# Kernel tuning notes

Measured on AMD Instinct MI355X. Metric: run time of the kernel, lower is better.

Reference implementation:

```python
import jax, jax.numpy as jnp
import numpy as np

N_NODES = 100000
N_EDGES = 3200000
D_IN = 128
D_H0 = 64
D_H1 = 32
N_GRAPHS = 1024
N_CLASSES = 16


def setup_inputs() -> dict:
    key = jax.random.key(0)
    ks = jax.random.split(key, 9)
    x = jax.random.normal(ks[0], (N_NODES, D_IN), dtype=jnp.float32)
    edge_index = jax.random.randint(ks[1], (2, N_EDGES), 0, N_NODES, dtype=jnp.int64)
    node_graph_index = jnp.sort(
        jax.random.randint(ks[2], (N_NODES,), 0, N_GRAPHS, dtype=jnp.int64))

    def glorot(k, shape):
        lim = np.sqrt(6.0 / (shape[0] + shape[1]))
        return jax.random.uniform(k, shape, jnp.float32, -lim, lim)

    W0 = glorot(ks[3], (D_IN, D_H0))
    b0 = jnp.zeros((D_H0,), jnp.float32)
    W1 = glorot(ks[4], (D_H0, D_H1))
    b1 = jnp.zeros((D_H1,), jnp.float32)
    Wd = glorot(ks[5], (D_H1, N_CLASSES))
    bd = jnp.zeros((N_CLASSES,), jnp.float32)
    return {"x": x, "edge_index": edge_index, "node_graph_index": node_graph_index,
            "W0": W0, "b0": b0, "W1": W1, "b1": b1, "Wd": Wd, "bd": bd}


def reference(x, edge_index, node_graph_index, W0, b0, W1, b1, Wd, bd):
    N = x.shape[0]
    # GCN renormalization: add self-loops, symmetric D^-1/2 (A+I) D^-1/2
    loops = jnp.arange(N, dtype=edge_index.dtype)
    row = jnp.concatenate([edge_index[0], loops])  # target nodes
    col = jnp.concatenate([edge_index[1], loops])  # source nodes
    deg = jax.ops.segment_sum(jnp.ones_like(row, dtype=x.dtype), row, num_segments=N)
    inv_sqrt = jax.lax.rsqrt(deg)  # deg >= 1 thanks to self-loops
    norm = inv_sqrt[row] * inv_sqrt[col]  # [E+N]

    def gcn(h, W, b):
        hW = h @ W                                   # [N, d_out]
        msg = hW[col] * norm[:, None]                # [E+N, d_out]
        agg = jax.ops.segment_sum(msg, row, num_segments=N)
        return jax.nn.relu(agg + b)

    h = gcn(x, W0, b0)          # [N, 64]  (dropout is identity at inference)
    h = gcn(h, W1, b1)          # [N, 32]

    # mean pool over graphs
    sums = jax.ops.segment_sum(h, node_graph_index, num_segments=N_GRAPHS)
    cnt = jax.ops.segment_sum(jnp.ones((N,), x.dtype), node_graph_index,
                              num_segments=N_GRAPHS)
    pooled = sums / jnp.maximum(cnt, 1.0)[:, None]   # [G, 32]
    return pooled @ Wd + bd                          # [G, n_classes]
```

## Files before the change

kernel.cpp:

```cpp
#include <hip/hip_runtime.h>

#define GSHIFT 8
#define GSIZE 256
#define MAXG 512
#define GCAP 8960
#define CHUNKA 8192

typedef unsigned short bfraw;

__device__ __forceinline__ bfraw f2bf(float f) {
    unsigned u = __float_as_uint(f);
    unsigned r = u + 0x7FFFu + ((u >> 16) & 1u);
    return (bfraw)(r >> 16);
}
__device__ __forceinline__ float bflo(unsigned u) { return __uint_as_float(u << 16); }
__device__ __forceinline__ float bfhi(unsigned u) { return __uint_as_float(u & 0xFFFF0000u); }


__global__ __launch_bounds__(512) void k_ginit(int* __restrict__ gcur, int ngroups) {
    int g = threadIdx.x;
    if (g < ngroups) gcur[g] = g * GCAP;
}

__global__ __launch_bounds__(512) void k_partA(const int* __restrict__ row,
                                               const int* __restrict__ col,
                                               int* __restrict__ gcur,
                                               int* __restrict__ gbuf,
                                               int E, int ngroups) {
    __shared__ int h[MAXG];
    __shared__ int lst[MAXG];
    __shared__ int base[MAXG];
    __shared__ int sorted[CHUNKA];
    __shared__ unsigned short gbin[CHUNKA];
    int tid = threadIdx.x;
    h[tid] = 0;
    int start = blockIdx.x * CHUNKA;
    int end = min(E, start + CHUNKA);
    int rr[16], cc[16];
#pragma unroll
    for (int q = 0; q < 4; ++q) {
        int i = start + tid * 4 + q * 2048;
        if (i + 3 < end) {
            int4 r4 = *(const int4*)(row + i);
            int4 c4 = *(const int4*)(col + i);
            rr[q * 4 + 0] = r4.x; rr[q * 4 + 1] = r4.y;
            rr[q * 4 + 2] = r4.z; rr[q * 4 + 3] = r4.w;
            cc[q * 4 + 0] = c4.x; cc[q * 4 + 1] = c4.y;
            cc[q * 4 + 2] = c4.z; cc[q * 4 + 3] = c4.w;
        } else {
#pragma unroll
            for (int j = 0; j < 4; ++j) {
                int idx = i + j;
                rr[q * 4 + j] = (idx < end) ? row[idx] : -1;
                cc[q * 4 + j] = (idx < end) ? col[idx] : 0;
            }
        }
    }
    __syncthreads();
#pragma unroll
    for (int j = 0; j < 16; ++j)
        if (rr[j] >= 0) atomicAdd(&h[rr[j] >> GSHIFT], 1);
    __syncthreads();
    int v = h[tid];
    lst[tid] = v;
    __syncthreads();
    for (int d = 1; d < MAXG; d <<= 1) {
        int a = (tid >= d) ? lst[tid - d] : 0;
        __syncthreads();
        lst[tid] += a;
        __syncthreads();
    }
    int excl = lst[tid] - v;
    base[tid] = (v > 0 && tid < ngroups) ? atomicAdd(&gcur[tid], v) : 0;
    lst[tid] = excl;
    h[tid] = excl;
    __syncthreads();
#pragma unroll
    for (int j = 0; j < 16; ++j) {
        int r = rr[j];
        if (r >= 0) {
            int g = r >> GSHIFT;
            int p = atomicAdd(&h[g], 1);
            sorted[p] = ((r & (GSIZE - 1)) << 17) | cc[j];
            gbin[p] = (unsigned short)g;
        }
    }
    __syncthreads();
    int cnt = end - start;
    for (int i = tid; i < cnt; i += 512) {
        int g = gbin[i];
        int dst = base[g] + (i - lst[g]);
        if (dst < (g + 1) * GCAP)
            gbuf[dst] = sorted[i];
    }
}

__global__ __launch_bounds__(512) void k_partB(const int* __restrict__ gbuf,
                                               const int* __restrict__ gcur,
                                               int* __restrict__ off,
                                               int* __restrict__ off2,
                                               int* __restrict__ scol,
                                               float* __restrict__ invs, int N) {
    __shared__ int hist[GSIZE];
    __shared__ int lex[GSIZE];
    __shared__ int sorted[GCAP];
    int g = blockIdx.x, tid = threadIdx.x;
    int s = g * GCAP;
    int cnt = min(gcur[g] - s, GCAP);
    if (tid < GSIZE) hist[tid] = 0;
    __syncthreads();
    for (int k = tid; k < cnt; k += 512)
        atomicAdd(&hist[gbuf[s + k] >> 17], 1);
    __syncthreads();
    int d0 = (tid < GSIZE) ? hist[tid] : 0;
    if (tid < GSIZE) lex[tid] = d0;
    __syncthreads();
    for (int d = 1; d < GSIZE; d <<= 1) {
        int a = 0;
        if (tid < GSIZE && tid >= d) a = lex[tid - d];
        __syncthreads();
        if (tid < GSIZE) lex[tid] += a;
        __syncthreads();
    }
    if (tid < GSIZE) {
        int excl = lex[tid] - d0;
        int node = (g << GSHIFT) + tid;
        if (node < N) {
            off[node] = s + excl;
            off2[node] = s + excl + d0;
            invs[node] = rsqrtf((float)(d0 + 1));
        }
        hist[tid] = excl;
    }
    __syncthreads();
    for (int k = tid; k < cnt; k += 512) {
        int p = gbuf[s + k];
        int pos = atomicAdd(&hist[p >> 17], 1);
        sorted[pos] = p & 0x1FFFF;
    }
    __syncthreads();
    for (int k = tid; k < cnt; k += 512) scol[s + k] = sorted[k];
}


__global__ __launch_bounds__(256) void k_gemm0(const float* __restrict__ x,
                                               const float* __restrict__ W,
                                               const float* __restrict__ invs,
                                               bfraw* __restrict__ out, int N) {
    __shared__ float sW[128 * 64];
    for (int i = threadIdx.x; i < 2048; i += 256)
        ((float4*)sW)[i] = ((const float4*)W)[i];
    __syncthreads();
    int t = threadIdx.x;
    int tc = t & 15, tr = t >> 4;
    int rbase = blockIdx.x * 64 + tr * 4;
    float acc[4][4] = {};
    int rr[4];
#pragma unroll
    for (int i = 0; i < 4; ++i) rr[i] = min(rbase + i, N - 1);
    for (int k = 0; k < 128; k += 4) {
        float4 wv0 = *(const float4*)&sW[(k + 0) * 64 + tc * 4];
        float4 wv1 = *(const float4*)&sW[(k + 1) * 64 + tc * 4];
        float4 wv2 = *(const float4*)&sW[(k + 2) * 64 + tc * 4];
        float4 wv3 = *(const float4*)&sW[(k + 3) * 64 + tc * 4];
#pragma unroll
        for (int i = 0; i < 4; ++i) {
            float4 xv = *(const float4*)(x + (size_t)rr[i] * 128 + k);
            acc[i][0] = fmaf(xv.x, wv0.x, acc[i][0]);
            acc[i][1] = fmaf(xv.x, wv0.y, acc[i][1]);
            acc[i][2] = fmaf(xv.x, wv0.z, acc[i][2]);
            acc[i][3] = fmaf(xv.x, wv0.w, acc[i][3]);
            acc[i][0] = fmaf(xv.y, wv1.x, acc[i][0]);
            acc[i][1] = fmaf(xv.y, wv1.y, acc[i][1]);
            acc[i][2] = fmaf(xv.y, wv1.z, acc[i][2]);
            acc[i][3] = fmaf(xv.y, wv1.w, acc[i][3]);
            acc[i][0] = fmaf(xv.z, wv2.x, acc[i][0]);
            acc[i][1] = fmaf(xv.z, wv2.y, acc[i][1]);
            acc[i][2] = fmaf(xv.z, wv2.z, acc[i][2]);
            acc[i][3] = fmaf(xv.z, wv2.w, acc[i][3]);
            acc[i][0] = fmaf(xv.w, wv3.x, acc[i][0]);
            acc[i][1] = fmaf(xv.w, wv3.y, acc[i][1]);
            acc[i][2] = fmaf(xv.w, wv3.z, acc[i][2]);
            acc[i][3] = fmaf(xv.w, wv3.w, acc[i][3]);
        }
    }
#pragma unroll
    for (int i = 0; i < 4; ++i) {
        int row = rbase + i;
        if (row < N) {
            float iv = invs[row];
            ushort4 o;
            o.x = f2bf(iv * acc[i][0]);
            o.y = f2bf(iv * acc[i][1]);
            o.z = f2bf(iv * acc[i][2]);
            o.w = f2bf(iv * acc[i][3]);
            *(ushort4*)(out + (size_t)row * 64 + tc * 4) = o;
        }
    }
}

__global__ __launch_bounds__(256) void k_gemm1(const float* __restrict__ h,
                                               const float* __restrict__ W,
                                               const float* __restrict__ invs,
                                               bfraw* __restrict__ out, int N) {
    __shared__ float sW[64 * 32];
    for (int i = threadIdx.x; i < 512; i += 256)
        ((float4*)sW)[i] = ((const float4*)W)[i];
    __syncthreads();
    int t = threadIdx.x;
    int tc = t & 7, tr = t >> 3;
    int rbase = blockIdx.x * 128 + tr * 4;
    float acc[4][4] = {};
    int rr[4];
#pragma unroll
    for (int i = 0; i < 4; ++i) rr[i] = min(rbase + i, N - 1);
    for (int k = 0; k < 64; k += 4) {
        float4 wv0 = *(const float4*)&sW[(k + 0) * 32 + tc * 4];
        float4 wv1 = *(const float4*)&sW[(k + 1) * 32 + tc * 4];
        float4 wv2 = *(const float4*)&sW[(k + 2) * 32 + tc * 4];
        float4 wv3 = *(const float4*)&sW[(k + 3) * 32 + tc * 4];
#pragma unroll
        for (int i = 0; i < 4; ++i) {
            float4 xv = *(const float4*)(h + (size_t)rr[i] * 64 + k);
            acc[i][0] = fmaf(xv.x, wv0.x, acc[i][0]);
            acc[i][1] = fmaf(xv.x, wv0.y, acc[i][1]);
            acc[i][2] = fmaf(xv.x, wv0.z, acc[i][2]);
            acc[i][3] = fmaf(xv.x, wv0.w, acc[i][3]);
            acc[i][0] = fmaf(xv.y, wv1.x, acc[i][0]);
            acc[i][1] = fmaf(xv.y, wv1.y, acc[i][1]);
            acc[i][2] = fmaf(xv.y, wv1.z, acc[i][2]);
            acc[i][3] = fmaf(xv.y, wv1.w, acc[i][3]);
            acc[i][0] = fmaf(xv.z, wv2.x, acc[i][0]);
            acc[i][1] = fmaf(xv.z, wv2.y, acc[i][1]);
            acc[i][2] = fmaf(xv.z, wv2.z, acc[i][2]);
            acc[i][3] = fmaf(xv.z, wv2.w, acc[i][3]);
            acc[i][0] = fmaf(xv.w, wv3.x, acc[i][0]);
            acc[i][1] = fmaf(xv.w, wv3.y, acc[i][1]);
            acc[i][2] = fmaf(xv.w, wv3.z, acc[i][2]);
            acc[i][3] = fmaf(xv.w, wv3.w, acc[i][3]);
        }
    }
#pragma unroll
    for (int i = 0; i < 4; ++i) {
        int row = rbase + i;
        if (row < N) {
            float iv = invs[row];
            ushort4 o;
            o.x = f2bf(iv * acc[i][0]);
            o.y = f2bf(iv * acc[i][1]);
            o.z = f2bf(iv * acc[i][2]);
            o.w = f2bf(iv * acc[i][3]);
            *(ushort4*)(out + (size_t)row * 32 + tc * 4) = o;
        }
    }
}


__global__ __launch_bounds__(256) void k_agg64_w(const int* __restrict__ scol,
                                                 const int* __restrict__ off,
                                                 const int* __restrict__ off2,
                                                 const float* __restrict__ invs,
                                                 const bfraw* __restrict__ hWb,
                                                 const float* __restrict__ bias,
                                                 float* __restrict__ h0, int N) {
    int node = blockIdx.x * 4 + (threadIdx.x >> 6);
    if (node >= N) return;
    int lane = threadIdx.x & 63;
    int fl = lane & 7, sg = lane >> 3;
    int s = off[node], e = off2[node];
    float a[8] = {}, c[8] = {};
    int k = s + sg;
    for (; k + 24 < e; k += 32) {
        int n0 = scol[k], n1 = scol[k + 8], n2 = scol[k + 16], n3 = scol[k + 24];
        uint4 u0 = *(const uint4*)(hWb + (size_t)n0 * 64 + fl * 8);
        uint4 u1 = *(const uint4*)(hWb + (size_t)n1 * 64 + fl * 8);
        uint4 u2 = *(const uint4*)(hWb + (size_t)n2 * 64 + fl * 8);
        uint4 u3 = *(const uint4*)(hWb + (size_t)n3 * 64 + fl * 8);
        a[0] += bflo(u0.x); a[1] += bfhi(u0.x); a[2] += bflo(u0.y); a[3] += bfhi(u0.y);
        a[4] += bflo(u0.z); a[5] += bfhi(u0.z); a[6] += bflo(u0.w); a[7] += bfhi(u0.w);
        c[0] += bflo(u1.x); c[1] += bfhi(u1.x); c[2] += bflo(u1.y); c[3] += bfhi(u1.y);
        c[4] += bflo(u1.z); c[5] += bfhi(u1.z); c[6] += bflo(u1.w); c[7] += bfhi(u1.w);
        a[0] += bflo(u2.x); a[1] += bfhi(u2.x); a[2] += bflo(u2.y); a[3] += bfhi(u2.y);
        a[4] += bflo(u2.z); a[5] += bfhi(u2.z); a[6] += bflo(u2.w); a[7] += bfhi(u2.w);
        c[0] += bflo(u3.x); c[1] += bfhi(u3.x); c[2] += bflo(u3.y); c[3] += bfhi(u3.y);
        c[4] += bflo(u3.z); c[5] += bfhi(u3.z); c[6] += bflo(u3.w); c[7] += bfhi(u3.w);
    }
    for (; k < e; k += 8) {
        uint4 u = *(const uint4*)(hWb + (size_t)scol[k] * 64 + fl * 8);
        a[0] += bflo(u.x); a[1] += bfhi(u.x); a[2] += bflo(u.y); a[3] += bfhi(u.y);
        a[4] += bflo(u.z); a[5] += bfhi(u.z); a[6] += bflo(u.w); a[7] += bfhi(u.w);
    }
#pragma unroll
    for (int j = 0; j < 8; ++j) a[j] += c[j];
#pragma unroll
    for (int m = 8; m < 64; m <<= 1) {
#pragma unroll
        for (int j = 0; j < 8; ++j) a[j] += __shfl_xor(a[j], m, 64);
    }
    if (sg == 0) {
        uint4 u = *(const uint4*)(hWb + (size_t)node * 64 + fl * 8);
        float iv = invs[node];
        int fb = fl * 8;
        float4 o1, o2;
        o1.x = fmaxf(iv * (a[0] + bflo(u.x)) + bias[fb + 0], 0.f);
        o1.y = fmaxf(iv * (a[1] + bfhi(u.x)) + bias[fb + 1], 0.f);
        o1.z = fmaxf(iv * (a[2] + bflo(u.y)) + bias[fb + 2], 0.f);
        o1.w = fmaxf(iv * (a[3] + bfhi(u.y)) + bias[fb + 3], 0.f);
        o2.x = fmaxf(iv * (a[4] + bflo(u.z)) + bias[fb + 4], 0.f);
        o2.y = fmaxf(iv * (a[5] + bfhi(u.z)) + bias[fb + 5], 0.f);
        o2.z = fmaxf(iv * (a[6] + bflo(u.w)) + bias[fb + 6], 0.f);
        o2.w = fmaxf(iv * (a[7] + bfhi(u.w)) + bias[fb + 7], 0.f);
        *(float4*)(h0 + (size_t)node * 64 + fb) = o1;
        *(float4*)(h0 + (size_t)node * 64 + fb + 4) = o2;
    }
}

__global__ __launch_bounds__(256) void k_agg32_w(const int* __restrict__ scol,
                                                 const int* __restrict__ off,
                                                 const int* __restrict__ off2,
                                                 const float* __restrict__ invs,
                                                 const bfraw* __restrict__ hWb,
                                                 const float* __restrict__ bias,
                                                 float* __restrict__ h1, int N) {
    int node = blockIdx.x * 4 + (threadIdx.x >> 6);
    if (node >= N) return;
    int lane = threadIdx.x & 63;
    int fl = lane & 3, sg = lane >> 2;
    int s = off[node], e = off2[node];
    float a[8] = {}, c[8] = {};
    int k = s + sg;
    for (; k + 16 < e; k += 32) {
        int n0 = scol[k], n1 = scol[k + 16];
        uint4 u0 = *(const uint4*)(hWb + (size_t)n0 * 32 + fl * 8);
        uint4 u1 = *(const uint4*)(hWb + (size_t)n1 * 32 + fl * 8);
        a[0] += bflo(u0.x); a[1] += bfhi(u0.x); a[2] += bflo(u0.y); a[3] += bfhi(u0.y);
        a[4] += bflo(u0.z); a[5] += bfhi(u0.z); a[6] += bflo(u0.w); a[7] += bfhi(u0.w);
        c[0] += bflo(u1.x); c[1] += bfhi(u1.x); c[2] += bflo(u1.y); c[3] += bfhi(u1.y);
        c[4] += bflo(u1.z); c[5] += bfhi(u1.z); c[6] += bflo(u1.w); c[7] += bfhi(u1.w);
    }
    for (; k < e; k += 16) {
        uint4 u = *(const uint4*)(hWb + (size_t)scol[k] * 32 + fl * 8);
        a[0] += bflo(u.x); a[1] += bfhi(u.x); a[2] += bflo(u.y); a[3] += bfhi(u.y);
        a[4] += bflo(u.z); a[5] += bfhi(u.z); a[6] += bflo(u.w); a[7] += bfhi(u.w);
    }
#pragma unroll
    for (int j = 0; j < 8; ++j) a[j] += c[j];
#pragma unroll
    for (int m = 4; m < 64; m <<= 1) {
#pragma unroll
        for (int j = 0; j < 8; ++j) a[j] += __shfl_xor(a[j], m, 64);
    }
    if (sg == 0) {
        uint4 u = *(const uint4*)(hWb + (size_t)node * 32 + fl * 8);
        float iv = invs[node];
        int fb = fl * 8;
        float4 o1, o2;
        o1.x = fmaxf(iv * (a[0] + bflo(u.x)) + bias[fb + 0], 0.f);
        o1.y = fmaxf(iv * (a[1] + bfhi(u.x)) + bias[fb + 1], 0.f);
        o1.z = fmaxf(iv * (a[2] + bflo(u.y)) + bias[fb + 2], 0.f);
        o1.w = fmaxf(iv * (a[3] + bfhi(u.y)) + bias[fb + 3], 0.f);
        o2.x = fmaxf(iv * (a[4] + bflo(u.z)) + bias[fb + 4], 0.f);
        o2.y = fmaxf(iv * (a[5] + bfhi(u.z)) + bias[fb + 5], 0.f);
        o2.z = fmaxf(iv * (a[6] + bflo(u.w)) + bias[fb + 6], 0.f);
        o2.w = fmaxf(iv * (a[7] + bfhi(u.w)) + bias[fb + 7], 0.f);
        *(float4*)(h1 + (size_t)node * 32 + fb) = o1;
        *(float4*)(h1 + (size_t)node * 32 + fb + 4) = o2;
    }
}


__global__ __launch_bounds__(256) void k_pool_head(const float* __restrict__ h1,
                                                   const int* __restrict__ gidx,
                                                   const float* __restrict__ Wd,
                                                   const float* __restrict__ bd,
                                                   float* __restrict__ out, int N) {
    int g = blockIdx.x;
    int tid = threadIdx.x;
    __shared__ int bound[2];
    if (tid < 2) {
        int target = g + tid;
        int lo = 0, hi = N;
        while (lo < hi) {
            int mid = (lo + hi) >> 1;
            if (gidx[mid] < target) lo = mid + 1; else hi = mid;
        }
        bound[tid] = lo;
    }
    __syncthreads();
    int s = bound[0], e = bound[1];
    int lane = tid & 63, w = tid >> 6;
    int f = lane & 31, half = lane >> 5;
    float acc = 0.f;
    for (int n = s + w * 2 + half; n < e; n += 8)
        acc += h1[(size_t)n * 32 + f];
    acc += __shfl_xor(acc, 32, 64);
    __shared__ float red[4][32];
    if (half == 0) red[w][f] = acc;
    __syncthreads();
    if (tid < 32) {
        float v = red[0][tid] + red[1][tid] + red[2][tid] + red[3][tid];
        red[0][tid] = v / fmaxf((float)(e - s), 1.0f);
    }
    __syncthreads();
    if (tid < 16) {
        float acc2 = bd[tid];
#pragma unroll
        for (int j = 0; j < 32; ++j)
            acc2 = fmaf(red[0][j], Wd[j * 16 + tid], acc2);
        out[g * 16 + tid] = acc2;
    }
}


static inline size_t align256(size_t v) { return (v + 255) & ~(size_t)255; }

extern "C" void kernel_launch(void* const* d_in, const int* in_sizes, int n_in,
                              void* d_out, int out_size, void* d_ws, size_t ws_size,
                              hipStream_t stream) {
    const float* x   = (const float*)d_in[0];
    const int*  erow = (const int*)d_in[1];
    const int*  gidx = (const int*)d_in[2];
    const float* W0  = (const float*)d_in[3];
    const float* b0  = (const float*)d_in[4];
    const float* W1  = (const float*)d_in[5];
    const float* b1  = (const float*)d_in[6];
    const float* Wd  = (const float*)d_in[7];
    const float* bd  = (const float*)d_in[8];
    float* out = (float*)d_out;

    const int E = in_sizes[1] / 2;
    const int* ecol = erow + E;
    const int N = in_sizes[2];
    const int G = out_size / 16;
    const int ngroups = (N + GSIZE - 1) / GSIZE;
    const int nchunks = (E + CHUNKA - 1) / CHUNKA;
    const size_t SLOTS = (size_t)ngroups * GCAP;

    char* ws = (char*)d_ws;
    size_t oInvs = 0;
    size_t oOff  = align256(oInvs + (size_t)N * 4);
    size_t oOff2 = align256(oOff + (size_t)N * 4);
    size_t oGc   = align256(oOff2 + (size_t)N * 4);
    size_t oScol = align256(oGc + (size_t)MAXG * 4);
    size_t oA    = align256(oScol + SLOTS * 4);
    size_t oB    = align256(oA + (size_t)N * 128);

    float* invs   = (float*)(ws + oInvs);
    int*   off    = (int*)(ws + oOff);
    int*   off2   = (int*)(ws + oOff2);
    int*   gcur   = (int*)(ws + oGc);
    int*   scol   = (int*)(ws + oScol);
    bfraw* tabA   = (bfraw*)(ws + oA);
    float* bufB   = (float*)(ws + oB);
    int*   gbuf   = (int*)bufB;
    float* h1     = bufB;

    k_ginit<<<1, 512, 0, stream>>>(gcur, ngroups);
    k_partA<<<nchunks, 512, 0, stream>>>(erow, ecol, gcur, gbuf, E, ngroups);
    k_partB<<<ngroups, 512, 0, stream>>>(gbuf, gcur, off, off2, scol, invs, N);

    k_gemm0<<<(N + 63) / 64, 256, 0, stream>>>(x, W0, invs, tabA, N);
    k_agg64_w<<<(N + 3) / 4, 256, 0, stream>>>(scol, off, off2, invs, tabA, b0, bufB, N);

    k_gemm1<<<(N + 127) / 128, 256, 0, stream>>>(bufB, W1, invs, tabA, N);
    k_agg32_w<<<(N + 3) / 4, 256, 0, stream>>>(scol, off, off2, invs, tabA, b1, h1, N);

    k_pool_head<<<G, 256, 0, stream>>>(h1, gidx, Wd, bd, out, N);
}
```

Measured before the change: 319.6 us.

## Fuse layer-1 GEMM into layer-0 aggregation epilogue and memset group counters

The layer-0 aggregation kernel now applies bias and ReLU, then multiplies the node's 64-wide hidden vector by W1 (held in padded shared memory) within the wavefront. It writes the scaled bf16 layer-1 table directly, which removes the separate gemm1 kernel and the fp32 h0 round trip through memory. The group counter init kernel is replaced by a memset, with the per-group base offset now added inside partA. The cost is that every block reloads W1 into LDS and each wave does extra shuffles and LDS reads.

```diff
diff --git a/kernel.cpp b/kernel.cpp
--- a/kernel.cpp
+++ b/kernel.cpp
@@ -16,11 +16,6 @@
 __device__ __forceinline__ float bflo(unsigned u) { return __uint_as_float(u << 16); }
 __device__ __forceinline__ float bfhi(unsigned u) { return __uint_as_float(u & 0xFFFF0000u); }
 
-
-__global__ __launch_bounds__(512) void k_ginit(int* __restrict__ gcur, int ngroups) {
-    int g = threadIdx.x;
-    if (g < ngroups) gcur[g] = g * GCAP;
-}
 
 __global__ __launch_bounds__(512) void k_partA(const int* __restrict__ row,
                                                const int* __restrict__ col,
@@ -71,7 +66,8 @@
         __syncthreads();
     }
     int excl = lst[tid] - v;
-    base[tid] = (v > 0 && tid < ngroups) ? atomicAdd(&gcur[tid], v) : 0;
+    base[tid] = (v > 0 && tid < ngroups)
+                    ? (tid * GCAP + atomicAdd(&gcur[tid], v)) : 0;
     lst[tid] = excl;
     h[tid] = excl;
     __syncthreads();
@@ -106,7 +102,7 @@
     __shared__ int sorted[GCAP];
     int g = blockIdx.x, tid = threadIdx.x;
     int s = g * GCAP;
-    int cnt = min(gcur[g] - s, GCAP);
+    int cnt = min(gcur[g], GCAP);
     if (tid < GSIZE) hist[tid] = 0;
     __syncthreads();
     for (int k = tid; k < cnt; k += 512)
@@ -199,70 +195,16 @@
     }
 }
 
-__global__ __launch_bounds__(256) void k_gemm1(const float* __restrict__ h,
-                                               const float* __restrict__ W,
-                                               const float* __restrict__ invs,
-                                               bfraw* __restrict__ out, int N) {
-    __shared__ float sW[64 * 32];
-    for (int i = threadIdx.x; i < 512; i += 256)
-        ((float4*)sW)[i] = ((const float4*)W)[i];
-    __syncthreads();
-    int t = threadIdx.x;
-    int tc = t & 7, tr = t >> 3;
-    int rbase = blockIdx.x * 128 + tr * 4;
-    float acc[4][4] = {};
-    int rr[4];
-#pragma unroll
-    for (int i = 0; i < 4; ++i) rr[i] = min(rbase + i, N - 1);
-    for (int k = 0; k < 64; k += 4) {
-        float4 wv0 = *(const float4*)&sW[(k + 0) * 32 + tc * 4];
-        float4 wv1 = *(const float4*)&sW[(k + 1) * 32 + tc * 4];
-        float4 wv2 = *(const float4*)&sW[(k + 2) * 32 + tc * 4];
-        float4 wv3 = *(const float4*)&sW[(k + 3) * 32 + tc * 4];
-#pragma unroll
-        for (int i = 0; i < 4; ++i) {
-            float4 xv = *(const float4*)(h + (size_t)rr[i] * 64 + k);
-            acc[i][0] = fmaf(xv.x, wv0.x, acc[i][0]);
-            acc[i][1] = fmaf(xv.x, wv0.y, acc[i][1]);
-            acc[i][2] = fmaf(xv.x, wv0.z, acc[i][2]);
-            acc[i][3] = fmaf(xv.x, wv0.w, acc[i][3]);
-            acc[i][0] = fmaf(xv.y, wv1.x, acc[i][0]);
-            acc[i][1] = fmaf(xv.y, wv1.y, acc[i][1]);
-            acc[i][2] = fmaf(xv.y, wv1.z, acc[i][2]);
-            acc[i][3] = fmaf(xv.y, wv1.w, acc[i][3]);
-            acc[i][0] = fmaf(xv.z, wv2.x, acc[i][0]);
-            acc[i][1] = fmaf(xv.z, wv2.y, acc[i][1]);
-            acc[i][2] = fmaf(xv.z, wv2.z, acc[i][2]);
-            acc[i][3] = fmaf(xv.z, wv2.w, acc[i][3]);
-            acc[i][0] = fmaf(xv.w, wv3.x, acc[i][0]);
-            acc[i][1] = fmaf(xv.w, wv3.y, acc[i][1]);
-            acc[i][2] = fmaf(xv.w, wv3.z, acc[i][2]);
-            acc[i][3] = fmaf(xv.w, wv3.w, acc[i][3]);
-        }
-    }
-#pragma unroll
-    for (int i = 0; i < 4; ++i) {
-        int row = rbase + i;
-        if (row < N) {
-            float iv = invs[row];
-            ushort4 o;
-            o.x = f2bf(iv * acc[i][0]);
-            o.y = f2bf(iv * acc[i][1]);
-            o.z = f2bf(iv * acc[i][2]);
-            o.w = f2bf(iv * acc[i][3]);
-            *(ushort4*)(out + (size_t)row * 32 + tc * 4) = o;
-        }
-    }
-}
-
-
-__global__ __launch_bounds__(256) void k_agg64_w(const int* __restrict__ scol,
-                                                 const int* __restrict__ off,
-                                                 const int* __restrict__ off2,
-                                                 const float* __restrict__ invs,
-                                                 const bfraw* __restrict__ hWb,
-                                                 const float* __restrict__ bias,
-                                                 float* __restrict__ h0, int N) {
+
+__global__ __launch_bounds__(256) void k_agg64_fused(
+        const int* __restrict__ scol, const int* __restrict__ off,
+        const int* __restrict__ off2, const float* __restrict__ invs,
+        const bfraw* __restrict__ hWb, const float* __restrict__ b0,
+        const float* __restrict__ W1, bfraw* __restrict__ tab1, int N) {
+    __shared__ float sW1[64 * 33];
+    for (int i = threadIdx.x; i < 2048; i += 256)
+        sW1[(i >> 5) * 33 + (i & 31)] = W1[i];
+    __syncthreads();
     int node = blockIdx.x * 4 + (threadIdx.x >> 6);
     if (node >= N) return;
     int lane = threadIdx.x & 63;
@@ -292,28 +234,55 @@
     }
 #pragma unroll
     for (int j = 0; j < 8; ++j) a[j] += c[j];
-#pragma unroll
-    for (int m = 8; m < 64; m <<= 1) {
-#pragma unroll
-        for (int j = 0; j < 8; ++j) a[j] += __shfl_xor(a[j], m, 64);
-    }
     if (sg == 0) {
         uint4 u = *(const uint4*)(hWb + (size_t)node * 64 + fl * 8);
-        float iv = invs[node];
-        int fb = fl * 8;
-        float4 o1, o2;
-        o1.x = fmaxf(iv * (a[0] + bflo(u.x)) + bias[fb + 0], 0.f);
-        o1.y = fmaxf(iv * (a[1] + bfhi(u.x)) + bias[fb + 1], 0.f);
-        o1.z = fmaxf(iv * (a[2] + bflo(u.y)) + bias[fb + 2], 0.f);
-        o1.w = fmaxf(iv * (a[3] + bfhi(u.y)) + bias[fb + 3], 0.f);
-        o2.x = fmaxf(iv * (a[4] + bflo(u.z)) + bias[fb + 4], 0.f);
-        o2.y = fmaxf(iv * (a[5] + bfhi(u.z)) + bias[fb + 5], 0.f);
-        o2.z = fmaxf(iv * (a[6] + bflo(u.w)) + bias[fb + 6], 0.f);
-        o2.w = fmaxf(iv * (a[7] + bfhi(u.w)) + bias[fb + 7], 0.f);
-        *(float4*)(h0 + (size_t)node * 64 + fb) = o1;
-        *(float4*)(h0 + (size_t)node * 64 + fb + 4) = o2;
-    }
-}
+        a[0] += bflo(u.x); a[1] += bfhi(u.x); a[2] += bflo(u.y); a[3] += bfhi(u.y);
+        a[4] += bflo(u.z); a[5] += bfhi(u.z); a[6] += bflo(u.w); a[7] += bfhi(u.w);
+    }
+#pragma unroll
+    for (int m = 8; m < 64; m <<= 1) {
+#pragma unroll
+        for (int j = 0; j < 8; ++j) a[j] += __shfl_xor(a[j], m, 64);
+    }
+    float iv = invs[node];
+    int fb = fl * 8;
+    float4 b0a = *(const float4*)(b0 + fb);
+    float4 b0b = *(const float4*)(b0 + fb + 4);
+    float hh[8];
+    hh[0] = fmaxf(iv * a[0] + b0a.x, 0.f);
+    hh[1] = fmaxf(iv * a[1] + b0a.y, 0.f);
+    hh[2] = fmaxf(iv * a[2] + b0a.z, 0.f);
+    hh[3] = fmaxf(iv * a[3] + b0a.w, 0.f);
+    hh[4] = fmaxf(iv * a[4] + b0b.x, 0.f);
+    hh[5] = fmaxf(iv * a[5] + b0b.y, 0.f);
+    hh[6] = fmaxf(iv * a[6] + b0b.z, 0.f);
+    hh[7] = fmaxf(iv * a[7] + b0b.w, 0.f);
+    float p0 = 0.f, p1 = 0.f, p2 = 0.f, p3 = 0.f;
+#pragma unroll
+    for (int j = 0; j < 8; ++j) {
+        float4 w = *(const float4*)&sW1[(fb + j) * 33 + sg * 4];
+        p0 = fmaf(hh[j], w.x, p0);
+        p1 = fmaf(hh[j], w.y, p1);
+        p2 = fmaf(hh[j], w.z, p2);
+        p3 = fmaf(hh[j], w.w, p3);
+    }
+#pragma unroll
+    for (int m = 1; m < 8; m <<= 1) {
+        p0 += __shfl_xor(p0, m, 64);
+        p1 += __shfl_xor(p1, m, 64);
+        p2 += __shfl_xor(p2, m, 64);
+        p3 += __shfl_xor(p3, m, 64);
+    }
+    if (fl == 0) {
+        ushort4 o;
+        o.x = f2bf(p0 * iv);
+        o.y = f2bf(p1 * iv);
+        o.z = f2bf(p2 * iv);
+        o.w = f2bf(p3 * iv);
+        *(ushort4*)(tab1 + (size_t)node * 32 + sg * 4) = o;
+    }
+}
+
 
 __global__ __launch_bounds__(256) void k_agg32_w(const int* __restrict__ scol,
                                                  const int* __restrict__ off,
@@ -444,6 +413,7 @@
     size_t oScol = align256(oGc + (size_t)MAXG * 4);
     size_t oA    = align256(oScol + SLOTS * 4);
     size_t oB    = align256(oA + (size_t)N * 128);
+    size_t oT1   = oB + align256(SLOTS * 4);
 
     float* invs   = (float*)(ws + oInvs);
     int*   off    = (int*)(ws + oOff);
@@ -453,17 +423,18 @@
     bfraw* tabA   = (bfraw*)(ws + oA);
     float* bufB   = (float*)(ws + oB);
     int*   gbuf   = (int*)bufB;
+    bfraw* tab1   = (bfraw*)(ws + oT1);
     float* h1     = bufB;
 
-    k_ginit<<<1, 512, 0, stream>>>(gcur, ngroups);
+    hipMemsetAsync(gcur, 0, (size_t)MAXG * 4, stream);
     k_partA<<<nchunks, 512, 0, stream>>>(erow, ecol, gcur, gbuf, E, ngroups);
     k_partB<<<ngroups, 512, 0, stream>>>(gbuf, gcur, off, off2, scol, invs, N);
 
     k_gemm0<<<(N + 63) / 64, 256, 0, stream>>>(x, W0, invs, tabA, N);
-    k_agg64_w<<<(N + 3) / 4, 256, 0, stream>>>(scol, off, off2, invs, tabA, b0, bufB, N);
-
-    k_gemm1<<<(N + 127) / 128, 256, 0, stream>>>(bufB, W1, invs, tabA, N);
-    k_agg32_w<<<(N + 3) / 4, 256, 0, stream>>>(scol, off, off2, invs, tabA, b1, h1, N);
+    k_agg64_fused<<<(N + 3) / 4, 256, 0, stream>>>(scol, off, off2, invs, tabA,
+                                                   b0, W1, tab1, N);
+
+    k_agg32_w<<<(N + 3) / 4, 256, 0, stream>>>(scol, off, off2, invs, tab1, b1, h1, N);
 
     k_pool_head<<<G, 256, 0, stream>>>(h1, gidx, Wd, bd, out, N);
 }
```

Result: slower. 338.3 us (+5.9%).
